# Optimization experiments

Measured on AMD Instinct MI355X. Metric: run time of the kernel, lower is better.

The kernel has to match this reference:

```python
import jax, jax.numpy as jnp
import numpy as np

N, E, HID, HEADS, EDIM = 32768, 262144, 64, 4, 3
C = HID  # per-head out channels (concat=False -> mean over heads)


def setup_inputs() -> dict:
    key = jax.random.key(0)
    ks = jax.random.split(key, 24)
    g = lambda k, shape, s=1.0: jax.random.normal(k, shape, jnp.float32) * s
    s_lin = 1.0 / np.sqrt(HID)
    s_edge = 1.0 / np.sqrt(EDIM)
    s_att = 1.0 / np.sqrt(C)
    inp = {
        "t": jnp.zeros((1,), jnp.float32),
        "h": g(ks[0], (N, HID)),
        "edge_index": jax.random.randint(ks[1], (2, E), 0, N, jnp.int32),
        "edge_attr": g(ks[2], (E, EDIM)),
        "W1": g(ks[3], (HID, HEADS * C), s_lin),
        "We1": g(ks[4], (EDIM, HEADS * C), s_edge),
        "att_src1": g(ks[5], (HEADS, C), s_att),
        "att_dst1": g(ks[6], (HEADS, C), s_att),
        "att_edge1": g(ks[7], (HEADS, C), s_att),
        "b1": jnp.zeros((C,), jnp.float32),
        "ln_g1": jnp.ones((HID,), jnp.float32),
        "ln_b1": jnp.zeros((HID,), jnp.float32),
        # last GAT layer's lin weight is scaled by 0.1 in __init__
        "W2": g(ks[8], (HID, HEADS * C), s_lin) * 0.1,
        "We2": g(ks[9], (EDIM, HEADS * C), s_edge),
        "att_src2": g(ks[10], (HEADS, C), s_att),
        "att_dst2": g(ks[11], (HEADS, C), s_att),
        "att_edge2": g(ks[12], (HEADS, C), s_att),
        "b2": jnp.zeros((C,), jnp.float32),
        "ln_g2": jnp.ones((HID,), jnp.float32),
        "ln_b2": jnp.zeros((HID,), jnp.float32),
    }
    return inp


def _gat_layer(z, src, dst, edge_attr, W, We, a_src, a_dst, a_edge, b):
    # PyG GATConv(edge_dim>0, concat=False, add_self_loops=False), eval mode (no dropout)
    x = (z @ W).reshape(-1, HEADS, C)                      # [N,H,C]
    alpha_s = jnp.einsum("nhc,hc->nh", x, a_src)           # [N,H]
    alpha_d = jnp.einsum("nhc,hc->nh", x, a_dst)           # [N,H]
    e = (edge_attr @ We).reshape(-1, HEADS, C)             # [E,H,C]
    alpha_e = jnp.einsum("ehc,hc->eh", e, a_edge)          # [E,H]
    logit = jax.nn.leaky_relu(alpha_s[src] + alpha_d[dst] + alpha_e, 0.2)  # [E,H]
    # segment softmax over incoming edges of each destination node
    m = jax.lax.stop_gradient(jax.ops.segment_max(logit, dst, num_segments=N))
    ex = jnp.exp(logit - m[dst])
    denom = jax.ops.segment_sum(ex, dst, num_segments=N)
    alpha = ex / (denom[dst] + 1e-16)                      # [E,H]
    msg = x[src] * alpha[..., None]                        # [E,H,C] gather + weight
    out = jax.ops.segment_sum(msg, dst, num_segments=N)    # [N,H,C] scatter-add
    return out.mean(axis=1) + b                            # head mean + bias -> [N,C]


def _layernorm(x, g, b, eps=1e-5):
    mu = x.mean(-1, keepdims=True)
    var = ((x - mu) ** 2).mean(-1, keepdims=True)
    return (x - mu) * jax.lax.rsqrt(var + eps) * g + b


def reference(t, h, edge_index, edge_attr, W1, We1, att_src1, att_dst1, att_edge1, b1,
              ln_g1, ln_b1, W2, We2, att_src2, att_dst2, att_edge2, b2, ln_g2, ln_b2):
    del t  # autonomous ODE func: t unused
    src, dst = edge_index[0], edge_index[1]
    z = h
    z = jax.nn.silu(_layernorm(_gat_layer(z, src, dst, edge_attr, W1, We1, att_src1, att_dst1, att_edge1, b1), ln_g1, ln_b1))
    z = jax.nn.silu(_layernorm(_gat_layer(z, src, dst, edge_attr, W2, We2, att_src2, att_dst2, att_edge2, b2), ln_g2, ln_b2))
    return z
```

## Files before the change

### kernel.cpp

```cpp
#include <hip/hip_runtime.h>
#include <math.h>

#define HIDDEN 64
#define HEADS 4
#define HC 256
#define CAP 64

typedef __attribute__((ext_vector_type(8))) short short8;
typedef __attribute__((ext_vector_type(4))) float f32x4;

__device__ __forceinline__ unsigned short f2bf(float f) {
    unsigned int u = __float_as_uint(f);
    u += 0x7fffu + ((u >> 16) & 1u);
    return (unsigned short)(u >> 16);
}

__device__ __forceinline__ unsigned short f2h(float f) {
    _Float16 h = (_Float16)f;
    return *(unsigned short*)&h;
}

__device__ __forceinline__ float h2f(unsigned int u) {
    unsigned short s = (unsigned short)u;
    _Float16 h = *(_Float16*)&s;
    return (float)h;
}

__device__ __forceinline__ float bflo(unsigned int u) { return __uint_as_float(u << 16); }
__device__ __forceinline__ float bfhi(unsigned int u) { return __uint_as_float(u & 0xffff0000u); }

__global__ __launch_bounds__(256) void k_fused(const int* __restrict__ dst,
                                               const int* __restrict__ src,
                                               const float* __restrict__ ea,
                                               const float* __restrict__ h,
                                               const float* __restrict__ W1f,
                                               const float* __restrict__ W2f,
                                               const float* __restrict__ We1,
                                               const float* __restrict__ ae1,
                                               const float* __restrict__ We2,
                                               const float* __restrict__ ae2,
                                               const float* __restrict__ ats1,
                                               const float* __restrict__ atd1,
                                               const float* __restrict__ ats2,
                                               const float* __restrict__ atd2,
                                               int* __restrict__ counts,
                                               uint2* __restrict__ eb,
                                               ushort* __restrict__ zb,
                                               ushort* __restrict__ wst1,
                                               ushort* __restrict__ wst2,
                                               float* __restrict__ wsv,
                                               float* __restrict__ wr, int E) {
    int t = threadIdx.x, b = blockIdx.x;
    if (b < 1024) {
        int e = b * 256 + t;
        if (e < E) {
            int d = dst[e];
            int c = atomicAdd(&counts[d], 1);
            if (c < CAP) {
                size_t slot = (size_t)d * CAP + c;
                unsigned int lo = (unsigned int)(src[e] & 0xffff)
                                | ((unsigned int)f2h(ea[e * 3 + 0]) << 16);
                unsigned int hi = (unsigned int)f2h(ea[e * 3 + 1])
                                | ((unsigned int)f2h(ea[e * 3 + 2]) << 16);
                eb[slot] = make_uint2(lo, hi);
            }
        }
    } else if (b < 3072) {
        int i = (b - 1024) * 256 + t;
        float4 v = ((const float4*)h)[i];
        ushort4 o;
        o.x = f2bf(v.x); o.y = f2bf(v.y); o.z = f2bf(v.z); o.w = f2bf(v.w);
        ((ushort4*)zb)[i] = o;
    } else if (b < 3200) {
        int j = (b - 3072) * 256 + t;
        const float* W = (j < 16384) ? W1f : W2f;
        ushort* wst = (j < 16384) ? wst1 : wst2;
        int i = j & 16383;
        int c = i >> 8, k = i & 255;
        wst[i] = f2bf(0.25f * W[(k & 63) * HC + (k >> 6) * 64 + c]);
    } else if (b < 3204) {
        int r = b - 3200;
        const float* W = (r >> 1) ? W2f : W1f;
        const float* at;
        if (r == 0) at = ats1; else if (r == 1) at = atd1;
        else if (r == 2) at = ats2; else at = atd2;
        int hh = t >> 6, k = t & 63;
        const float4* wrow = (const float4*)&W[k * HC + hh * 64];
        const float4* arow = (const float4*)&at[hh * 64];
        float v = 0.f;
#pragma unroll
        for (int c4 = 0; c4 < 16; ++c4) {
            float4 wv = wrow[c4], av = arow[c4];
            v += wv.x * av.x + wv.y * av.y + wv.z * av.z + wv.w * av.w;
        }
        wsv[r * 256 + hh * 64 + k] = v;
    } else {
        int wv = t >> 6, lane = t & 63;
#pragma unroll
        for (int it = 0; it < 6; ++it) {
            int comb = wv + it * 4;
            int layer = comb / 12;
            int dh = comb % 12;
            int d = dh >> 2, hh = dh & 3;
            const float* We = layer ? We2 : We1;
            const float* at = layer ? ae2 : ae1;
            float v = We[d * HC + hh * HIDDEN + lane] * at[hh * HIDDEN + lane];
            for (int o = 32; o > 0; o >>= 1) v += __shfl_down(v, o);
            if (lane == 0) wr[layer * 16 + d * HEADS + hh] = v;
        }
    }
}

__global__ __launch_bounds__(256) void k_alpha(const ushort* __restrict__ zb,
                                               const float* __restrict__ wsv,
                                               float* __restrict__ as_,
                                               float* __restrict__ ad_) {
    __shared__ float ls[512];
    int t = threadIdx.x;
    ls[t] = wsv[t];
    ls[t + 256] = wsv[t + 256];
    __syncthreads();
    int n = blockIdx.x * 256 + t;
    const ushort* zr = zb + (size_t)n * HIDDEN;
    float as[4] = {0.f, 0.f, 0.f, 0.f};
    float ad[4] = {0.f, 0.f, 0.f, 0.f};
#pragma unroll
    for (int ks = 0; ks < 8; ++ks) {
        uint4 v = *(const uint4*)(zr + ks * 8);
        unsigned int uu[4] = {v.x, v.y, v.z, v.w};
#pragma unroll
        for (int p = 0; p < 4; ++p) {
            float f0 = bflo(uu[p]), f1 = bfhi(uu[p]);
            int k = ks * 8 + p * 2;
#pragma unroll
            for (int hh = 0; hh < 4; ++hh) {
                as[hh] += f0 * ls[hh * 64 + k] + f1 * ls[hh * 64 + k + 1];
                ad[hh] += f0 * ls[256 + hh * 64 + k] + f1 * ls[256 + hh * 64 + k + 1];
            }
        }
    }
    *(float4*)&as_[n * 4] = make_float4(as[0], as[1], as[2], as[3]);
    *(float4*)&ad_[n * 4] = make_float4(ad[0], ad[1], ad[2], ad[3]);
}

__global__ __launch_bounds__(256, 4) void k_aggout(
        const ushort* __restrict__ zb, const uint2* __restrict__ eb,
        const int* __restrict__ counts,
        const float* __restrict__ as_, const float* __restrict__ ad_,
        const float* __restrict__ wrl,
        const ushort* __restrict__ wst, const float* __restrict__ bias,
        const float* __restrict__ lng, const float* __restrict__ lnb,
        const float* __restrict__ wsv2,
        float* __restrict__ as2, float* __restrict__ ad2,
        float* __restrict__ outf, ushort* __restrict__ outb, int N) {
    __shared__ ushort sagg[16][264];
    int lane = threadIdx.x & 63;
    int wave = threadIdx.x >> 6;
    int h = lane >> 4, sub = lane & 15;
    int nbase = blockIdx.x * 16;

    float w0 = wrl[h], w1 = wrl[4 + h], w2 = wrl[8 + h];

    int degs[4]; float ad4s[4];
#pragma unroll
    for (int i = 0; i < 4; ++i) {
        int n = nbase + wave * 4 + i;
        int d = counts[n];
        degs[i] = (d > CAP) ? CAP : d;
        ad4s[i] = ad_[(size_t)n * 4 + h];
    }

#pragma unroll
    for (int i = 0; i < 4; ++i) {
        int nl = wave * 4 + i;
        int n = nbase + nl;
        int deg = degs[i];
        size_t base = (size_t)n * CAP;
        float ad4 = ad4s[i];
        float ssum = 0.f;
        float acc[4][4];
#pragma unroll
        for (int a = 0; a < 4; ++a)
#pragma unroll
            for (int j = 0; j < 4; ++j) acc[a][j] = 0.f;

        for (int cs = 0; cs < deg; cs += 16) {
            int idx = cs + sub;
            int s_sub = 0;
            float wgt = 0.f;
            if (idx < deg) {
                uint2 rec = eb[base + idx];
                s_sub = (int)(rec.x & 0xffffu);
                float lg = as_[(size_t)s_sub * 4 + h] + ad4
                         + h2f(rec.x >> 16) * w0
                         + h2f(rec.y) * w1
                         + h2f(rec.y >> 16) * w2;
                lg = (lg >= 0.f) ? lg : 0.2f * lg;
                wgt = __expf(lg);
            }
            ssum += wgt;

            int jb = deg - cs; if (jb > 16) jb = 16;
            for (int j4 = 0; j4 < jb; j4 += 4) {
                int eidx = j4 + h;
                int s_g = __shfl(s_sub, eidx);
                uint2 zv = *(const uint2*)&zb[(size_t)s_g * HIDDEN + sub * 4];
                float z0 = bflo(zv.x), z1 = bfhi(zv.x);
                float z2v = bflo(zv.y), z3 = bfhi(zv.y);
#pragma unroll
                for (int hh = 0; hh < 4; ++hh) {
                    float wh = __shfl(wgt, hh * 16 + eidx);
                    acc[hh][0] += wh * z0;
                    acc[hh][1] += wh * z1;
                    acc[hh][2] += wh * z2v;
                    acc[hh][3] += wh * z3;
                }
            }
        }
#pragma unroll
        for (int o = 1; o < 16; o <<= 1) ssum += __shfl_xor(ssum, o);
        float winv = 1.f / (ssum + 1e-16f);
#pragma unroll
        for (int a = 0; a < 4; ++a)
#pragma unroll
            for (int j = 0; j < 4; ++j) {
                acc[a][j] += __shfl_xor(acc[a][j], 16);
                acc[a][j] += __shfl_xor(acc[a][j], 32);
            }
        float sel[4];
#pragma unroll
        for (int j = 0; j < 4; ++j)
            sel[j] = (h == 0) ? acc[0][j] : (h == 1) ? acc[1][j]
                   : (h == 2) ? acc[2][j] : acc[3][j];
        uint2 pk;
        pk.x = (unsigned)f2bf(sel[0] * winv) | ((unsigned)f2bf(sel[1] * winv) << 16);
        pk.y = (unsigned)f2bf(sel[2] * winv) | ((unsigned)f2bf(sel[3] * winv) << 16);
        *(uint2*)&sagg[nl][h * 64 + sub * 4] = pk;
    }
    __syncthreads();

    if (wave == 0) {
        int q = lane & 15, quad = lane >> 4;
        short8 a[8];
#pragma unroll
        for (int ks = 0; ks < 8; ++ks)
            a[ks] = *(const short8*)&sagg[q][quad * 8 + ks * 32];

        f32x4 acc[4];
#pragma unroll
        for (int nt = 0; nt < 4; ++nt) {
            const ushort* brow = wst + (size_t)(nt * 16 + q) * HC + quad * 8;
            f32x4 c4 = {0.f, 0.f, 0.f, 0.f};
#pragma unroll
            for (int ks = 0; ks < 8; ++ks) {
                short8 bfr = *(const short8*)(brow + ks * 32);
                c4 = __builtin_amdgcn_mfma_f32_16x16x32_bf16(a[ks], bfr, c4, 0, 0, 0);
            }
            acc[nt] = c4;
        }

        float u[4][4], s1[4] = {0.f, 0.f, 0.f, 0.f};
#pragma unroll
        for (int nt = 0; nt < 4; ++nt) {
            float bv = bias[nt * 16 + q];
#pragma unroll
            for (int r = 0; r < 4; ++r) { u[nt][r] = acc[nt][r] + bv; s1[r] += u[nt][r]; }
        }
#pragma unroll
        for (int o = 1; o < 16; o <<= 1)
#pragma unroll
            for (int r = 0; r < 4; ++r) s1[r] += __shfl_xor(s1[r], o);
        float mu[4], s2[4] = {0.f, 0.f, 0.f, 0.f};
#pragma unroll
        for (int r = 0; r < 4; ++r) mu[r] = s1[r] * (1.f / 64.f);
#pragma unroll
        for (int nt = 0; nt < 4; ++nt)
#pragma unroll
            for (int r = 0; r < 4; ++r) { float d = u[nt][r] - mu[r]; s2[r] += d * d; }
#pragma unroll
        for (int o = 1; o < 16; o <<= 1)
#pragma unroll
            for (int r = 0; r < 4; ++r) s2[r] += __shfl_xor(s2[r], o);
        float rstd[4];
#pragma unroll
        for (int r = 0; r < 4; ++r) rstd[r] = rsqrtf(s2[r] * (1.f / 64.f) + 1e-5f);

        float rv[4][4];
#pragma unroll
        for (int nt = 0; nt < 4; ++nt) {
            float gv = lng[nt * 16 + q], bb = lnb[nt * 16 + q];
#pragma unroll
            for (int r = 0; r < 4; ++r) {
                float y = (u[nt][r] - mu[r]) * rstd[r] * gv + bb;
                rv[nt][r] = y / (1.f + __expf(-y));
            }
        }

        if (outb) {
#pragma unroll
            for (int nt = 0; nt < 4; ++nt)
#pragma unroll
                for (int r = 0; r < 4; ++r)
                    outb[(size_t)(nbase + quad * 4 + r) * HIDDEN + nt * 16 + q] = f2bf(rv[nt][r]);
            float vs[4][4] = {{0.f}}, vd[4][4] = {{0.f}};
#pragma unroll
            for (int hh = 0; hh < 4; ++hh)
#pragma unroll
                for (int nt = 0; nt < 4; ++nt) {
                    float wsc = wsv2[hh * 64 + nt * 16 + q];
                    float wdc = wsv2[256 + hh * 64 + nt * 16 + q];
#pragma unroll
                    for (int r = 0; r < 4; ++r) {
                        vs[r][hh] += rv[nt][r] * wsc;
                        vd[r][hh] += rv[nt][r] * wdc;
                    }
                }
#pragma unroll
            for (int o = 1; o < 16; o <<= 1)
#pragma unroll
                for (int r = 0; r < 4; ++r)
#pragma unroll
                    for (int hh = 0; hh < 4; ++hh) {
                        vs[r][hh] += __shfl_xor(vs[r][hh], o);
                        vd[r][hh] += __shfl_xor(vd[r][hh], o);
                    }
            if (q < 4) {
#pragma unroll
                for (int r = 0; r < 4; ++r) {
                    float sv = (q == 0) ? vs[r][0] : (q == 1) ? vs[r][1]
                             : (q == 2) ? vs[r][2] : vs[r][3];
                    float dv = (q == 0) ? vd[r][0] : (q == 1) ? vd[r][1]
                             : (q == 2) ? vd[r][2] : vd[r][3];
                    int n = nbase + quad * 4 + r;
                    as2[(size_t)n * 4 + q] = sv;
                    ad2[(size_t)n * 4 + q] = dv;
                }
            }
        } else {
#pragma unroll
            for (int nt = 0; nt < 4; ++nt)
#pragma unroll
                for (int r = 0; r < 4; ++r)
                    outf[(size_t)(nbase + quad * 4 + r) * HIDDEN + nt * 16 + q] = rv[nt][r];
        }
    }
}


extern "C" void kernel_launch(void* const* d_in, const int* in_sizes, int n_in,
                              void* d_out, int out_size, void* d_ws, size_t ws_size,
                              hipStream_t stream) {
    const float* h   = (const float*)d_in[1];
    const int*   ei  = (const int*)d_in[2];
    const float* ea  = (const float*)d_in[3];
    const float* W1  = (const float*)d_in[4];
    const float* We1 = (const float*)d_in[5];
    const float* as1 = (const float*)d_in[6];
    const float* ad1 = (const float*)d_in[7];
    const float* ae1 = (const float*)d_in[8];
    const float* b1  = (const float*)d_in[9];
    const float* lg1 = (const float*)d_in[10];
    const float* lb1 = (const float*)d_in[11];
    const float* W2  = (const float*)d_in[12];
    const float* We2 = (const float*)d_in[13];
    const float* as2 = (const float*)d_in[14];
    const float* ad2 = (const float*)d_in[15];
    const float* ae2 = (const float*)d_in[16];
    const float* b2  = (const float*)d_in[17];
    const float* lg2 = (const float*)d_in[18];
    const float* lb2 = (const float*)d_in[19];

    const int N = in_sizes[1] / HIDDEN;
    const int E = in_sizes[2] / 2;
    const int* srcp = ei;
    const int* dstp = ei + E;

    char* w = (char*)d_ws;
    ushort* zb    = (ushort*)w; w += (size_t)N * HIDDEN * 2;
    ushort* zb2   = (ushort*)w; w += (size_t)N * HIDDEN * 2;
    float* as_    = (float*)w;  w += (size_t)N * HEADS * 4;
    float* adv    = (float*)w;  w += (size_t)N * HEADS * 4;
    float* as2_   = (float*)w;  w += (size_t)N * HEADS * 4;
    float* ad2_   = (float*)w;  w += (size_t)N * HEADS * 4;
    ushort* wst1  = (ushort*)w; w += 16384 * 2;
    ushort* wst2  = (ushort*)w; w += 16384 * 2;
    float* wsv    = (float*)w;  w += 1024 * 4;
    float* wr     = (float*)w;  w += 128;
    int* counts   = (int*)w;    w += (size_t)N * 4;
    uint2* eb     = (uint2*)w;  w += (size_t)N * CAP * 8;

    hipMemsetAsync(counts, 0, (size_t)N * 4, stream);
    k_fused<<<3205, 256, 0, stream>>>(dstp, srcp, ea, h, W1, W2,
                                      We1, ae1, We2, ae2,
                                      as1, ad1, as2, ad2,
                                      counts, eb, zb, wst1, wst2, wsv, wr, E);

    k_alpha<<<N / 256, 256, 0, stream>>>(zb, wsv, as_, adv);

    k_aggout<<<N / 16, 256, 0, stream>>>(zb, eb, counts, as_, adv, wr,
                                         wst1, b1, lg1, lb1, wsv + 512,
                                         as2_, ad2_, nullptr, zb2, N);
    k_aggout<<<N / 16, 256, 0, stream>>>(zb2, eb, counts, as2_, ad2_, wr + 16,
                                         wst2, b2, lg2, lb2, nullptr,
                                         nullptr, nullptr, (float*)d_out, nullptr, N);
}
```

Baseline: 189.5 us.

## Spread aggout epilogue GEMM+LayerNorm across all four waves, move alpha2 to separate kernel

The epilogue of the aggregation kernel previously ran only on wave 0, which did all four 16-column MFMA tiles, the LayerNorm, and the next layer's attention-logit projection while the other three waves sat idle. Now each of the four waves computes one 16-column tile. LayerNorm partial sums (sum and sum of squares) are combined across waves through shared memory with an extra barrier. The fused layer-2 alpha projection is removed and replaced by an extra k_alpha launch on the bf16 intermediate, which adds a kernel launch and a reread of zb2. The variance is now computed as E[x^2]-mu^2, which is slightly less numerically robust than the two-pass form.

```diff
diff --git a/kernel.cpp b/kernel.cpp
--- a/kernel.cpp
+++ b/kernel.cpp
@@ -150,10 +150,9 @@
         const float* __restrict__ wrl,
         const ushort* __restrict__ wst, const float* __restrict__ bias,
         const float* __restrict__ lng, const float* __restrict__ lnb,
-        const float* __restrict__ wsv2,
-        float* __restrict__ as2, float* __restrict__ ad2,
         float* __restrict__ outf, ushort* __restrict__ outb, int N) {
     __shared__ ushort sagg[16][264];
+    __shared__ float pst[16][4][2];
     int lane = threadIdx.x & 63;
     int wave = threadIdx.x >> 6;
     int h = lane >> 4, sub = lane & 15;
@@ -239,109 +238,61 @@
     }
     __syncthreads();
 
-    if (wave == 0) {
-        int q = lane & 15, quad = lane >> 4;
-        short8 a[8];
-#pragma unroll
-        for (int ks = 0; ks < 8; ++ks)
-            a[ks] = *(const short8*)&sagg[q][quad * 8 + ks * 32];
-
-        f32x4 acc[4];
-#pragma unroll
-        for (int nt = 0; nt < 4; ++nt) {
-            const ushort* brow = wst + (size_t)(nt * 16 + q) * HC + quad * 8;
-            f32x4 c4 = {0.f, 0.f, 0.f, 0.f};
-#pragma unroll
-            for (int ks = 0; ks < 8; ++ks) {
-                short8 bfr = *(const short8*)(brow + ks * 32);
-                c4 = __builtin_amdgcn_mfma_f32_16x16x32_bf16(a[ks], bfr, c4, 0, 0, 0);
-            }
-            acc[nt] = c4;
-        }
-
-        float u[4][4], s1[4] = {0.f, 0.f, 0.f, 0.f};
-#pragma unroll
-        for (int nt = 0; nt < 4; ++nt) {
-            float bv = bias[nt * 16 + q];
-#pragma unroll
-            for (int r = 0; r < 4; ++r) { u[nt][r] = acc[nt][r] + bv; s1[r] += u[nt][r]; }
-        }
-#pragma unroll
-        for (int o = 1; o < 16; o <<= 1)
-#pragma unroll
-            for (int r = 0; r < 4; ++r) s1[r] += __shfl_xor(s1[r], o);
-        float mu[4], s2[4] = {0.f, 0.f, 0.f, 0.f};
-#pragma unroll
-        for (int r = 0; r < 4; ++r) mu[r] = s1[r] * (1.f / 64.f);
-#pragma unroll
-        for (int nt = 0; nt < 4; ++nt)
-#pragma unroll
-            for (int r = 0; r < 4; ++r) { float d = u[nt][r] - mu[r]; s2[r] += d * d; }
-#pragma unroll
-        for (int o = 1; o < 16; o <<= 1)
-#pragma unroll
-            for (int r = 0; r < 4; ++r) s2[r] += __shfl_xor(s2[r], o);
-        float rstd[4];
-#pragma unroll
-        for (int r = 0; r < 4; ++r) rstd[r] = rsqrtf(s2[r] * (1.f / 64.f) + 1e-5f);
-
-        float rv[4][4];
-#pragma unroll
-        for (int nt = 0; nt < 4; ++nt) {
-            float gv = lng[nt * 16 + q], bb = lnb[nt * 16 + q];
-#pragma unroll
-            for (int r = 0; r < 4; ++r) {
-                float y = (u[nt][r] - mu[r]) * rstd[r] * gv + bb;
-                rv[nt][r] = y / (1.f + __expf(-y));
-            }
-        }
-
+    int q = sub, quad = h;
+    int col = wave * 16 + q;
+    float bv = bias[col];
+    float gv = lng[col], bb = lnb[col];
+
+    short8 a[8];
+#pragma unroll
+    for (int ks = 0; ks < 8; ++ks)
+        a[ks] = *(const short8*)&sagg[q][quad * 8 + ks * 32];
+
+    const ushort* brow = wst + (size_t)col * HC + quad * 8;
+    f32x4 c4 = {0.f, 0.f, 0.f, 0.f};
+#pragma unroll
+    for (int ks = 0; ks < 8; ++ks) {
+        short8 bfr = *(const short8*)(brow + ks * 32);
+        c4 = __builtin_amdgcn_mfma_f32_16x16x32_bf16(a[ks], bfr, c4, 0, 0, 0);
+    }
+
+    float u[4], s1[4], ss[4];
+#pragma unroll
+    for (int r = 0; r < 4; ++r) {
+        u[r] = c4[r] + bv;
+        s1[r] = u[r];
+        ss[r] = u[r] * u[r];
+    }
+#pragma unroll
+    for (int o = 1; o < 16; o <<= 1)
+#pragma unroll
+        for (int r = 0; r < 4; ++r) {
+            s1[r] += __shfl_xor(s1[r], o);
+            ss[r] += __shfl_xor(ss[r], o);
+        }
+    if (q == 0) {
+#pragma unroll
+        for (int r = 0; r < 4; ++r) {
+            pst[quad * 4 + r][wave][0] = s1[r];
+            pst[quad * 4 + r][wave][1] = ss[r];
+        }
+    }
+    __syncthreads();
+
+#pragma unroll
+    for (int r = 0; r < 4; ++r) {
+        int row = quad * 4 + r;
+        float t1 = pst[row][0][0] + pst[row][1][0] + pst[row][2][0] + pst[row][3][0];
+        float t2 = pst[row][0][1] + pst[row][1][1] + pst[row][2][1] + pst[row][3][1];
+        float mu = t1 * (1.f / 64.f);
+        float var = t2 * (1.f / 64.f) - mu * mu;
+        float rstd = rsqrtf(var + 1e-5f);
+        float y = (u[r] - mu) * rstd * gv + bb;
+        float rv = y / (1.f + __expf(-y));
         if (outb) {
-#pragma unroll
-            for (int nt = 0; nt < 4; ++nt)
-#pragma unroll
-                for (int r = 0; r < 4; ++r)
-                    outb[(size_t)(nbase + quad * 4 + r) * HIDDEN + nt * 16 + q] = f2bf(rv[nt][r]);
-            float vs[4][4] = {{0.f}}, vd[4][4] = {{0.f}};
-#pragma unroll
-            for (int hh = 0; hh < 4; ++hh)
-#pragma unroll
-                for (int nt = 0; nt < 4; ++nt) {
-                    float wsc = wsv2[hh * 64 + nt * 16 + q];
-                    float wdc = wsv2[256 + hh * 64 + nt * 16 + q];
-#pragma unroll
-                    for (int r = 0; r < 4; ++r) {
-                        vs[r][hh] += rv[nt][r] * wsc;
-                        vd[r][hh] += rv[nt][r] * wdc;
-                    }
-                }
-#pragma unroll
-            for (int o = 1; o < 16; o <<= 1)
-#pragma unroll
-                for (int r = 0; r < 4; ++r)
-#pragma unroll
-                    for (int hh = 0; hh < 4; ++hh) {
-                        vs[r][hh] += __shfl_xor(vs[r][hh], o);
-                        vd[r][hh] += __shfl_xor(vd[r][hh], o);
-                    }
-            if (q < 4) {
-#pragma unroll
-                for (int r = 0; r < 4; ++r) {
-                    float sv = (q == 0) ? vs[r][0] : (q == 1) ? vs[r][1]
-                             : (q == 2) ? vs[r][2] : vs[r][3];
-                    float dv = (q == 0) ? vd[r][0] : (q == 1) ? vd[r][1]
-                             : (q == 2) ? vd[r][2] : vd[r][3];
-                    int n = nbase + quad * 4 + r;
-                    as2[(size_t)n * 4 + q] = sv;
-                    ad2[(size_t)n * 4 + q] = dv;
-                }
-            }
+            outb[(size_t)(nbase + row) * HIDDEN + col] = f2bf(rv);
         } else {
-#pragma unroll
-            for (int nt = 0; nt < 4; ++nt)
-#pragma unroll
-                for (int r = 0; r < 4; ++r)
-                    outf[(size_t)(nbase + quad * 4 + r) * HIDDEN + nt * 16 + q] = rv[nt][r];
+            outf[(size_t)(nbase + row) * HIDDEN + col] = rv;
         }
     }
 }
@@ -396,11 +347,9 @@
                                       counts, eb, zb, wst1, wst2, wsv, wr, E);
 
     k_alpha<<<N / 256, 256, 0, stream>>>(zb, wsv, as_, adv);
-
     k_aggout<<<N / 16, 256, 0, stream>>>(zb, eb, counts, as_, adv, wr,
-                                         wst1, b1, lg1, lb1, wsv + 512,
-                                         as2_, ad2_, nullptr, zb2, N);
+                                         wst1, b1, lg1, lb1, nullptr, zb2, N);
+    k_alpha<<<N / 256, 256, 0, stream>>>(zb2, wsv + 512, as2_, ad2_);
     k_aggout<<<N / 16, 256, 0, stream>>>(zb2, eb, counts, as2_, ad2_, wr + 16,
-                                         wst2, b2, lg2, lb2, nullptr,
-                                         nullptr, nullptr, (float*)d_out, nullptr, N);
-}
+                                         wst2, b2, lg2, lb2, (float*)d_out, nullptr, N);
+}
```

After: 191.8 us. About the same (+1.2%).
